# Optimization experiments

Hardware: AMD Instinct MI355X
Metric: run time of the kernel (lower is better)

The kernel has to match this reference:

```python
import jax, jax.numpy as jnp
import numpy as np

B, A = 8192, 16
HID, NK, NQ, NV = 256, 32, 32, 128
IN_DIM, CUR_HID, CUR_OUT, N_ACT = 512, 512, 128, 64
EXT_LAMBD, INT_LAMBD = 1.0, 0.5


def setup_inputs() -> dict:
    key = jax.random.key(0)
    ks = jax.random.split(key, 16)
    def w(k, i, o):
        return jax.random.normal(k, (i, o), jnp.float32) / np.sqrt(i)
    return {
        'x': jax.random.normal(ks[0], (B * A, IN_DIM), jnp.float32),
        'hidden': jax.random.normal(ks[1], (B, A, HID), jnp.float32),
        'Wk': w(ks[2], HID, NK), 'bk': jnp.zeros((NK,), jnp.float32),
        'Wv': w(ks[3], HID, NV), 'bv': jnp.zeros((NV,), jnp.float32),
        'Wq': w(ks[4], HID, NQ), 'bq': jnp.zeros((NQ,), jnp.float32),
        'Wa': w(ks[5], NQ + NK * A, A), 'ba': jnp.zeros((A,), jnp.float32),
        'Wt1': w(ks[6], IN_DIM, CUR_HID), 'bt1': jnp.zeros((CUR_HID,), jnp.float32),
        'Wt2': w(ks[7], CUR_HID, CUR_OUT), 'bt2': jnp.zeros((CUR_OUT,), jnp.float32),
        'Wp1': w(ks[8], IN_DIM, CUR_HID), 'bp1': jnp.zeros((CUR_HID,), jnp.float32),
        'Wp2': w(ks[9], CUR_HID, CUR_HID), 'bp2': jnp.zeros((CUR_HID,), jnp.float32),
        'Wp3': w(ks[10], CUR_HID, CUR_OUT), 'bp3': jnp.zeros((CUR_OUT,), jnp.float32),
        'Wc': w(ks[11], NV + HID, HID), 'bc': jnp.zeros((HID,), jnp.float32),
        'W2': w(ks[12], HID, N_ACT), 'b2': jnp.zeros((N_ACT,), jnp.float32),
    }


def _aggregate(x, hidden, Wk, bk, Wv, bv, Wq, bq, Wa, ba, Wt1, bt1, Wt2, bt2,
               Wp1, bp1, Wp2, bp2, Wp3, bp3, Wc, bc, W2, b2):
    # communicate(): per-agent key / value / query projections
    key_ = hidden @ Wk + bk          # [B, A, NK]
    value = hidden @ Wv + bv         # [B, A, NV]
    query = hidden @ Wq + bq         # [B, A, NQ]
    # torch.cat([key[:, i, :] for i in range(A)], -1) == reshape; repeat == broadcast
    flat_key = key_.reshape(B, A * NK)
    qk = jnp.concatenate(
        [query, jnp.broadcast_to(flat_key[:, None, :], (B, A, A * NK))], axis=-1)
    attn_weights = jax.nn.softmax(qk @ Wa + ba, axis=-1)   # [B, A, A]
    # intrinsic-motivation predictors (dropout p=0.5 in eval mode -> identity)
    tar = jax.nn.relu(x @ Wt1 + bt1) @ Wt2 + bt2           # [B*A, CUR_OUT]
    pred = jax.nn.relu(x @ Wp1 + bp1)
    pred = jax.nn.relu(pred @ Wp2 + bp2)
    pred = pred @ Wp3 + bp3
    int_imp = jnp.mean((tar - pred) ** 2, axis=-1).reshape(B, A)
    int_imp = jax.nn.softmax(int_imp, axis=-1)             # [B, A]
    # view(B,A,1).repeat(1,1,A).permute(0,2,1): out[b,i,j] = int_imp[b,j]
    int_mat = jnp.broadcast_to(int_imp[:, None, :], (B, A, A))
    attn = EXT_LAMBD * attn_weights + INT_LAMBD * jax.lax.stop_gradient(int_mat)
    applied = jnp.einsum('bij,bjv->biv', attn, value)      # [B, A, NV]
    comb = jax.nn.relu(jnp.concatenate([applied, hidden], axis=-1) @ Wc + bc)
    return comb @ W2 + b2                                  # [B, A, N_ACT]


def reference(x, hidden, Wk, bk, Wv, bv, Wq, bq, Wa, ba, Wt1, bt1, Wt2, bt2,
              Wp1, bp1, Wp2, bp2, Wp3, bp3, Wc, bc, W2, b2):
    return _aggregate(x, hidden, Wk, bk, Wv, bv, Wq, bq, Wa, ba, Wt1, bt1,
                      Wt2, bt2, Wp1, bp1, Wp2, bp2, Wp3, bp3, Wc, bc, W2, b2)
```

## Files before the change

### kernel.cpp

```cpp
#include <hip/hip_runtime.h>
#include <cstddef>
#include <cstdint>

typedef unsigned short ushort_t;
typedef __attribute__((ext_vector_type(4))) float f32x4;
typedef __attribute__((ext_vector_type(8))) short bf16x8;

#define BB   8192
#define AA   16
#define BA   131072

__device__ __forceinline__ float bf2f(ushort_t u) {
    union { float f; uint32_t i; } v; v.i = ((uint32_t)u) << 16; return v.f;
}
__device__ __forceinline__ ushort_t f2bf(float f) {
    union { float f; uint32_t i; } v; v.f = f;
    uint32_t r = v.i + 0x7fffu + ((v.i >> 16) & 1u);
    return (ushort_t)(r >> 16);
}
__device__ __forceinline__ void gload_lds16(const void* g, void* l) {
    __builtin_amdgcn_global_load_lds(
        (const __attribute__((address_space(1))) uint32_t*)g,
        (__attribute__((address_space(3))) uint32_t*)l, 16, 0, 0);
}

template<bool RELU>
__global__ __launch_bounds__(512, 2)
void gemm8p(const ushort_t* __restrict__ A, int lda,
            const ushort_t* __restrict__ A2, int lda2, int ksplit,
            const ushort_t* __restrict__ Bt,
            const float* __restrict__ bias,
            ushort_t* __restrict__ C, int ldc, int K, int lgx, int rpx)
{
    __shared__ ushort_t lds[65536];

    const int tid  = threadIdx.x;
    const int w    = tid >> 6;
    const int lane = tid & 63;
    const int wm   = w >> 2;
    const int wn   = w & 3;
    const int fr   = lane & 15;
    const int fq   = lane >> 4;

    const int bid  = blockIdx.x;
    const int xcd  = bid & 7;
    const int slot = bid >> 3;
    const int x    = slot & ((1 << lgx) - 1);
    const int y    = xcd * rpx + (slot >> lgx);
    const size_t brow = (size_t)y * 256;
    const int    bcol = x * 256;

    const int NT = K >> 6;
    const int NI = NT >> 1;

    const int srl = tid >> 3;
    const int spg = tid & 7;

    f32x4 acc[8][4];
#pragma unroll
    for (int m = 0; m < 8; ++m)
#pragma unroll
        for (int n = 0; n < 4; ++n) acc[m][n] = (f32x4){0.f, 0.f, 0.f, 0.f};

    auto stageA = [&](int T, int s, int bi) {
        const int k0  = T << 6;
        const int row = (srl < 32) ? s * 32 + srl : 128 + s * 32 + (srl - 32);
        const int col = ((spg ^ (row & 7)) << 3);
        const ushort_t* src;
        if (k0 >= ksplit) src = A2 + (brow + row) * (size_t)lda2 + (k0 - ksplit) + col;
        else              src = A  + (brow + row) * (size_t)lda  + k0 + col;
        gload_lds16(src, &lds[(bi << 15) + row * 64 + spg * 8]);
    };
    auto stageB = [&](int T, int c, int bi) {
        const int k0  = T << 6;
        const int row = c * 64 + srl;
        const int col = ((spg ^ (row & 7)) << 3);
        gload_lds16(Bt + (size_t)(bcol + row) * K + k0 + col,
                    &lds[(bi << 15) + 16384 + row * 64 + spg * 8]);
    };

    stageA(0, 0, 0); stageB(0, 0, 0);
    stageA(0, 1, 0); stageB(0, 1, 0);
    stageA(0, 2, 0); stageB(0, 2, 0);
    stageA(0, 3, 0); stageB(0, 3, 0);
    stageA(1, 0, 1); stageB(1, 0, 1);
    stageA(1, 1, 1); stageB(1, 1, 1);
    stageA(1, 2, 1); stageB(1, 2, 1);

    bf16x8 breg[4][2];

    for (int i = 0; i < NI; ++i) {
        const bool more = (i + 1 < NI);
#pragma unroll
        for (int h = 0; h < 2; ++h) {
            const int bufA = h << 15;
            const int bufB = (h << 15) + 16384;
#pragma unroll
            for (int q = 0; q < 4; ++q) {
                if (q == 0) {
                    if (h == 0 || more) asm volatile("s_waitcnt vmcnt(6)" ::: "memory");
                    else                asm volatile("s_waitcnt vmcnt(0)" ::: "memory");
                    __builtin_amdgcn_sched_barrier(0);
                    __builtin_amdgcn_s_barrier();
#pragma unroll
                    for (int n = 0; n < 4; ++n)
#pragma unroll
                        for (int kk = 0; kk < 2; ++kk) {
                            const int row = wn * 64 + n * 16 + fr;
                            const int gp  = ((kk * 4 + fq) ^ (row & 7)) << 3;
                            breg[n][kk] = *(const bf16x8*)&lds[bufB + row * 64 + gp];
                        }
                }
                bf16x8 areg[2][2];
#pragma unroll
                for (int j = 0; j < 2; ++j)
#pragma unroll
                    for (int kk = 0; kk < 2; ++kk) {
                        const int row = wm * 128 + (2 * q + j) * 16 + fr;
                        const int gp  = ((kk * 4 + fq) ^ (row & 7)) << 3;
                        areg[j][kk] = *(const bf16x8*)&lds[bufA + row * 64 + gp];
                    }
                if (h == 0) {
                    if (q == 0)      { stageA(2*i+1, 3, 1); stageB(2*i+1, 3, 1); }
                    else if (more)   { stageA(2*i+2, q-1, 0); stageB(2*i+2, q-1, 0); }
                } else {
                    if (q == 0) { if (more) { stageA(2*i+2, 3, 0); stageB(2*i+2, 3, 0); } }
                    else        { if (more) { stageA(2*i+3, q-1, 1); stageB(2*i+3, q-1, 1); } }
                }
                __builtin_amdgcn_s_barrier();
                __builtin_amdgcn_s_setprio(1);
#pragma unroll
                for (int j = 0; j < 2; ++j)
#pragma unroll
                    for (int n = 0; n < 4; ++n)
#pragma unroll
                        for (int kk = 0; kk < 2; ++kk)
                            acc[2*q+j][n] = __builtin_amdgcn_mfma_f32_16x16x32_bf16(
                                areg[j][kk], breg[n][kk], acc[2*q+j][n], 0, 0, 0);
                __builtin_amdgcn_s_setprio(0);
                __builtin_amdgcn_s_barrier();
            }
        }
    }

#pragma unroll
    for (int m = 0; m < 8; ++m) {
        const size_t rowb = brow + wm * 128 + m * 16 + fq * 4;
#pragma unroll
        for (int n = 0; n < 4; ++n) {
            const int col = bcol + wn * 64 + n * 16 + fr;
            const float bv = bias[col];
#pragma unroll
            for (int r = 0; r < 4; ++r) {
                float v = acc[m][n][r] + bv;
                if (RELU) v = fmaxf(v, 0.f);
                C[(rowb + r) * (size_t)ldc + col] = f2bf(v);
            }
        }
    }
}

template<bool OBF16, bool RELU>
__global__ __launch_bounds__(256)
void gemm_mfma(const ushort_t* __restrict__ A, int lda,
               const ushort_t* __restrict__ A2, int lda2, int ksplit,
               const ushort_t* __restrict__ Bt,
               const float* __restrict__ bias,
               void* __restrict__ C, int ldc, int N, int K, int lgx)
{
    __shared__ ushort_t As[2][128 * 64];
    __shared__ ushort_t Bs[2][128 * 64];

    const int tid  = threadIdx.x;
    const int w    = tid >> 6;
    const int lane = tid & 63;
    const int wm   = w >> 1;
    const int wn   = w & 1;

    const int bid  = blockIdx.x;
    const int xcd  = bid & 7;
    const int slot = bid >> 3;
    const int x    = slot & ((1 << lgx) - 1);
    const int y    = xcd * 128 + (slot >> lgx);
    const size_t brow = (size_t)y * 128;
    const int    bcol = x * 128;

    const int fr   = lane & 15;
    const int fq   = lane >> 4;
    const int srow = lane >> 3;
    const int scol = (lane & 7) << 3;

    f32x4 acc[4][4];
#pragma unroll
    for (int i = 0; i < 4; ++i)
#pragma unroll
        for (int j = 0; j < 4; ++j) acc[i][j] = (f32x4){0.f, 0.f, 0.f, 0.f};

    const int NT = K >> 6;

    auto stage = [&](int buf, int k0) {
#pragma unroll
        for (int i = 0; i < 4; ++i) {
            const int c = (w << 2) + i;
            const int r = (c << 3) + srow;
            const ushort_t* asrc;
            if (k0 >= ksplit)
                asrc = A2 + (brow + r) * (size_t)lda2 + (k0 - ksplit) + scol;
            else
                asrc = A  + (brow + r) * (size_t)lda  + k0 + scol;
            gload_lds16(asrc, &As[buf][(c << 9) + lane * 8]);
            gload_lds16(Bt + (size_t)(bcol + r) * K + k0 + scol,
                        &Bs[buf][(c << 9) + lane * 8]);
        }
    };

    stage(0, 0);
    __syncthreads();

    for (int t = 0; t < NT; ++t) {
        const int cur = t & 1;
        if (t + 1 < NT) stage(cur ^ 1, (t + 1) << 6);
#pragma unroll
        for (int kk = 0; kk < 2; ++kk) {
            bf16x8 a[4], b[4];
#pragma unroll
            for (int f = 0; f < 4; ++f) {
                a[f] = *(const bf16x8*)&As[cur][(wm * 64 + f * 16 + fr) * 64 + kk * 32 + fq * 8];
                b[f] = *(const bf16x8*)&Bs[cur][(wn * 64 + f * 16 + fr) * 64 + kk * 32 + fq * 8];
            }
#pragma unroll
            for (int fm = 0; fm < 4; ++fm)
#pragma unroll
                for (int fn = 0; fn < 4; ++fn)
                    acc[fm][fn] = __builtin_amdgcn_mfma_f32_16x16x32_bf16(
                        a[fm], b[fn], acc[fm][fn], 0, 0, 0);
        }
        __syncthreads();
    }

#pragma unroll
    for (int fm = 0; fm < 4; ++fm) {
        const size_t rowb = brow + wm * 64 + fm * 16 + fq * 4;
#pragma unroll
        for (int fn = 0; fn < 4; ++fn) {
            const int col = bcol + wn * 64 + fn * 16 + fr;
            if (col < N) {
                const float bv = bias[col];
#pragma unroll
                for (int r = 0; r < 4; ++r) {
                    float v = acc[fm][fn][r] + bv;
                    if (RELU) v = fmaxf(v, 0.f);
                    const size_t idx = (rowb + r) * (size_t)ldc + col;
                    if (OBF16) ((ushort_t*)C)[idx] = f2bf(v);
                    else       ((float*)C)[idx]    = v;
                }
            }
        }
    }
}

__global__ __launch_bounds__(256)
void transpose_w(const float* __restrict__ W, ushort_t* __restrict__ Wt,
                 int K, int N, int Npad)
{
    int idx = blockIdx.x * 256 + threadIdx.x;
    if (idx >= Npad * K) return;
    int n = idx / K, k = idx - n * K;
    float v = (n < N) ? W[(size_t)k * N + n] : 0.f;
    Wt[idx] = f2bf(v);
}

__global__ __launch_bounds__(256)
void transpose_wk(const float* __restrict__ W, ushort_t* __restrict__ Wt,
                  int Ksrc, int N, int ldk, int kOff, float sign)
{
    int idx = blockIdx.x * 256 + threadIdx.x;
    if (idx >= N * Ksrc) return;
    int n = idx / Ksrc, k = idx - n * Ksrc;
    Wt[(size_t)n * ldk + kOff + k] = f2bf(sign * W[(size_t)k * N + n]);
}

__global__ __launch_bounds__(256)
void conv_f32_bf16(const float* __restrict__ src, ushort_t* __restrict__ dst)
{
    size_t q = (size_t)blockIdx.x * 256 + threadIdx.x;
    float4 v = ((const float4*)src)[q];
    ushort_t* d = dst + q * 4;
    d[0] = f2bf(v.x); d[1] = f2bf(v.y); d[2] = f2bf(v.z); d[3] = f2bf(v.w);
}

__global__ __launch_bounds__(256)
void fill_zero(ushort_t* __restrict__ p, int n)
{
    int i = blockIdx.x * 256 + threadIdx.x;
    if (i < n) p[i] = 0;
}

__global__ void pack_cat2(const float* __restrict__ a, const float* __restrict__ b,
                          float* __restrict__ o)
{
    int j = blockIdx.x * 256 + threadIdx.x;
    if (j < 512) o[j] = a[j];
    else if (j < 1024) o[j] = b[j - 512];
}

__global__ void pack_bias(const float* __restrict__ bk, const float* __restrict__ bq,
                          const float* __restrict__ bv, float* __restrict__ pb)
{
    int j = threadIdx.x;
    float v = 0.f;
    if      (j < 32)  v = bk[j];
    else if (j < 64)  v = bq[j - 32];
    else if (j < 192) v = bv[j - 64];
    pb[j] = v;
}

__global__ void make_cbias(const float* __restrict__ bt2, const float* __restrict__ bp3,
                           float* __restrict__ cb)
{
    int j = threadIdx.x;
    cb[j] = (j < 128) ? (bt2[j] - bp3[j]) : 0.f;
}

__global__ __launch_bounds__(64)
void mse_softmax(const ushort_t* __restrict__ diff, float* __restrict__ int_imp)
{
    const int b = blockIdx.x, lane = threadIdx.x;
    __shared__ float m[AA];
    for (int a = 0; a < AA; ++a) {
        const uint32_t u = *(const uint32_t*)(diff + ((size_t)b * AA + a) * 256 + lane * 2);
        float d0 = bf2f((ushort_t)(u & 0xffff));
        float d1 = bf2f((ushort_t)(u >> 16));
        float s = d0 * d0 + d1 * d1;
#pragma unroll
        for (int off = 32; off > 0; off >>= 1) s += __shfl_down(s, off);
        if (lane == 0) m[a] = s * (1.f / 128.f);
    }
    __syncthreads();
    if (lane == 0) {
        float mx = -1e30f;
#pragma unroll
        for (int a = 0; a < AA; ++a) mx = fmaxf(mx, m[a]);
        float e[AA], den = 0.f;
#pragma unroll
        for (int a = 0; a < AA; ++a) { e[a] = __expf(m[a] - mx); den += e[a]; }
        float inv = 1.f / den;
#pragma unroll
        for (int a = 0; a < AA; ++a) int_imp[(size_t)b * AA + a] = e[a] * inv;
    }
}

__global__ __launch_bounds__(256)
void attn_apply(const ushort_t* __restrict__ kvq, const float* __restrict__ Wa,
                const float* __restrict__ ba, const float* __restrict__ iimp,
                ushort_t* __restrict__ applied)
{
    const int b = blockIdx.x, t = threadIdx.x;
    __shared__ float klds[512], qlds[512];
    __shared__ ushort_t vlds[2048];
    __shared__ float part[16][17];
    __shared__ float kp[16];
    __shared__ float attn[16][17];

    for (int i = t; i < 512; i += 256) {
        int a = i >> 5, c = i & 31;
        const size_t base = ((size_t)b * AA + a) * 256;
        klds[i] = bf2f(kvq[base + c]);
        qlds[i] = bf2f(kvq[base + 32 + c]);
    }
    for (int i = t; i < 2048; i += 256) {
        int j = i >> 7, v = i & 127;
        vlds[i] = kvq[((size_t)b * AA + j) * 256 + 64 + v];
    }
    __syncthreads();

    {
        int j = t & 15, seg = t >> 4;
        float s = 0.f;
        for (int c = seg * 32; c < seg * 32 + 32; ++c)
            s += klds[c] * Wa[(32 + c) * 16 + j];
        part[j][seg] = s;
    }
    __syncthreads();
    if (t < 16) {
        float s = 0.f;
#pragma unroll
        for (int seg = 0; seg < 16; ++seg) s += part[t][seg];
        kp[t] = s;
    }
    __syncthreads();

    {
        int i = t >> 4, j = t & 15;
        float s = 0.f;
#pragma unroll
        for (int q = 0; q < 32; ++q) s += qlds[i * 32 + q] * Wa[q * 16 + j];
        attn[i][j] = s + kp[j] + ba[j];
    }
    __syncthreads();
    if (t < 16) {
        float mx = -1e30f;
#pragma unroll
        for (int j = 0; j < 16; ++j) mx = fmaxf(mx, attn[t][j]);
        float e[16], den = 0.f;
#pragma unroll
        for (int j = 0; j < 16; ++j) { e[j] = __expf(attn[t][j] - mx); den += e[j]; }
        float inv = 1.f / den;
#pragma unroll
        for (int j = 0; j < 16; ++j)
            attn[t][j] = e[j] * inv + 0.5f * iimp[b * 16 + j];
    }
    __syncthreads();

    for (int o = t; o < 2048; o += 256) {
        int i = o >> 7, v = o & 127;
        float s = 0.f;
#pragma unroll
        for (int j = 0; j < 16; ++j) s += attn[i][j] * bf2f(vlds[j * 128 + v]);
        applied[((size_t)b * AA + i) * 128 + v] = f2bf(s);
    }
}

extern "C" void kernel_launch(void* const* d_in, const int* in_sizes, int n_in,
                              void* d_out, int out_size, void* d_ws, size_t ws_size,
                              hipStream_t stream)
{
    const float* x      = (const float*)d_in[0];
    const float* hidden = (const float*)d_in[1];
    const float* Wk  = (const float*)d_in[2];
    const float* bk  = (const float*)d_in[3];
    const float* Wv  = (const float*)d_in[4];
    const float* bv  = (const float*)d_in[5];
    const float* Wq  = (const float*)d_in[6];
    const float* bq  = (const float*)d_in[7];
    const float* Wa  = (const float*)d_in[8];
    const float* ba  = (const float*)d_in[9];
    const float* Wt1 = (const float*)d_in[10];
    const float* bt1 = (const float*)d_in[11];
    const float* Wt2 = (const float*)d_in[12];
    const float* bt2 = (const float*)d_in[13];
    const float* Wp1 = (const float*)d_in[14];
    const float* bp1 = (const float*)d_in[15];
    const float* Wp2 = (const float*)d_in[16];
    const float* bp2 = (const float*)d_in[17];
    const float* Wp3 = (const float*)d_in[18];
    const float* bp3 = (const float*)d_in[19];
    const float* Wc  = (const float*)d_in[20];
    const float* bc  = (const float*)d_in[21];
    const float* W2  = (const float*)d_in[22];
    const float* b2  = (const float*)d_in[23];

    float*    out = (float*)d_out;
    ushort_t* ws  = (ushort_t*)d_ws;

    ushort_t* xb  = ws;
    ushort_t* ht2 = xb + (size_t)BA * 512;
    ushort_t* hp2 = ht2 + (size_t)BA * 1024;
    ushort_t* WT  = hp2 + (size_t)BA * 512;
    ushort_t* diff    = xb;
    ushort_t* kvq     = xb + (size_t)BA * 256;
    ushort_t* hiddenb = hp2;
    ushort_t* applied = ht2;
    ushort_t* comb    = ht2 + (size_t)BA * 128;

    ushort_t* Bg1  = WT;
    ushort_t* Wp2t = Bg1  + 1024 * 512;
    ushort_t* Dt   = Wp2t + 512 * 512;
    ushort_t* Wkvq = Dt   + 256 * 1024;
    ushort_t* Wct  = Wkvq + 256 * 256;
    ushort_t* W2t  = Wct  + 256 * 384;
    float* g1bias = (float*)(W2t + 128 * 256);
    float* pbias  = g1bias + 1024;
    float* cbias  = pbias + 256;
    float* iimp   = cbias + 256;

    const dim3 blk(256);
    const int BIG = 1 << 30;

    transpose_w<<<1024, blk, 0, stream>>>(Wt1, Bg1,             512, 512, 512);
    transpose_w<<<1024, blk, 0, stream>>>(Wp1, Bg1 + 512 * 512, 512, 512, 512);
    transpose_w<<<1024, blk, 0, stream>>>(Wp2, Wp2t, 512, 512, 512);
    transpose_wk<<<256, blk, 0, stream>>>(Wt2, Dt, 512, 128, 1024, 0,    1.f);
    transpose_wk<<<256, blk, 0, stream>>>(Wp3, Dt, 512, 128, 1024, 512, -1.f);
    fill_zero<<<512, blk, 0, stream>>>(Dt + 128 * 1024, 128 * 1024);
    transpose_w<<<32,  blk, 0, stream>>>(Wk, Wkvq + 0 * 256,   256, 32, 32);
    transpose_w<<<32,  blk, 0, stream>>>(Wq, Wkvq + 32 * 256,  256, 32, 32);
    transpose_w<<<128, blk, 0, stream>>>(Wv, Wkvq + 64 * 256,  256, 128, 128);
    transpose_w<<<64,  blk, 0, stream>>>(Wk, Wkvq + 192 * 256, 256, 0, 64);
    transpose_w<<<384, blk, 0, stream>>>(Wc, Wct, 384, 256, 256);
    transpose_w<<<128, blk, 0, stream>>>(W2, W2t, 256, 64, 128);
    pack_cat2<<<4, 256, 0, stream>>>(bt1, bp1, g1bias);
    pack_bias<<<1, 256, 0, stream>>>(bk, bq, bv, pbias);
    make_cbias<<<1, 256, 0, stream>>>(bt2, bp3, cbias);

    conv_f32_bf16<<<65536, blk, 0, stream>>>(x, xb);
    gemm8p<true><<<2048, 512, 0, stream>>>(
        xb, 512, xb, 512, BIG, Bg1, g1bias, ht2, 1024, 512, 2, 64);
    gemm8p<true><<<1024, 512, 0, stream>>>(
        ht2 + 512, 1024, ht2 + 512, 1024, BIG, Wp2t, bp2, hp2, 512, 512, 1, 64);
    gemm8p<false><<<512, 512, 0, stream>>>(
        ht2, 1024, hp2, 512, 512, Dt, cbias, diff, 256, 1024, 0, 64);
    mse_softmax<<<BB, 64, 0, stream>>>(diff, iimp);

    conv_f32_bf16<<<32768, blk, 0, stream>>>(hidden, hiddenb);
    gemm8p<false><<<512, 512, 0, stream>>>(
        hiddenb, 256, hiddenb, 256, BIG, Wkvq, pbias, kvq, 256, 256, 0, 64);
    attn_apply<<<BB, blk, 0, stream>>>(kvq, Wa, ba, iimp, applied);

    gemm8p<true><<<512, 512, 0, stream>>>(
        applied, 128, hiddenb, 256, 128, Wct, bc, comb, 256, 384, 0, 64);
    gemm_mfma<false, false><<<1024, blk, 0, stream>>>(
        comb, 256, comb, 256, BIG, W2t, b2, out, 64, 64, 256, 0);
}
```

Baseline: 645.5 us.

## Fuse MSE-softmax and attention apply into GEMM epilogues

Adds epilogue modes to the 256x256 MFMA GEMM. One mode reduces the curiosity difference rows to squared-error means and applies the per-batch softmax inside the GEMM. The other keeps the K/Q/V tile in LDS, computes the attention logits, softmax and value mixing, and writes the applied tensor directly. This removes two standalone kernels and the global round-trips of the diff and kvq buffers. The cost is more LDS use and serial scalar epilogue work inside the GEMM blocks, and the launch-bounds occupancy hint is dropped.

```diff
diff --git a/kernel.cpp b/kernel.cpp
--- a/kernel.cpp
+++ b/kernel.cpp
@@ -24,13 +24,15 @@
         (__attribute__((address_space(3))) uint32_t*)l, 16, 0, 0);
 }
 
-template<bool RELU>
-__global__ __launch_bounds__(512, 2)
+template<int MODE, bool RELU>
+__global__ __launch_bounds__(512)
 void gemm8p(const ushort_t* __restrict__ A, int lda,
             const ushort_t* __restrict__ A2, int lda2, int ksplit,
             const ushort_t* __restrict__ Bt,
             const float* __restrict__ bias,
-            ushort_t* __restrict__ C, int ldc, int K, int lgx, int rpx)
+            ushort_t* __restrict__ C, int ldc, int K, int lgx, int rpx,
+            const float* __restrict__ Wa, const float* __restrict__ ba,
+            const float* __restrict__ iimp_in, float* __restrict__ iimp_out)
 {
     __shared__ ushort_t lds[65536];
 
@@ -143,18 +145,145 @@
         }
     }
 
-#pragma unroll
-    for (int m = 0; m < 8; ++m) {
-        const size_t rowb = brow + wm * 128 + m * 16 + fq * 4;
-#pragma unroll
-        for (int n = 0; n < 4; ++n) {
-            const int col = bcol + wn * 64 + n * 16 + fr;
-            const float bv = bias[col];
+    if (MODE == 0) {
+#pragma unroll
+        for (int m = 0; m < 8; ++m) {
+            const size_t rowb = brow + wm * 128 + m * 16 + fq * 4;
+#pragma unroll
+            for (int n = 0; n < 4; ++n) {
+                const int col = bcol + wn * 64 + n * 16 + fr;
+                const float bv = bias[col];
+#pragma unroll
+                for (int r = 0; r < 4; ++r) {
+                    float v = acc[m][n][r] + bv;
+                    if (RELU) v = fmaxf(v, 0.f);
+                    C[(rowb + r) * (size_t)ldc + col] = f2bf(v);
+                }
+            }
+        }
+    }
+
+    if (MODE == 1) {
+        float* rowsq = (float*)lds;
+        if (tid < 256) rowsq[tid] = 0.f;
+        __syncthreads();
+#pragma unroll
+        for (int m = 0; m < 8; ++m) {
 #pragma unroll
             for (int r = 0; r < 4; ++r) {
-                float v = acc[m][n][r] + bv;
-                if (RELU) v = fmaxf(v, 0.f);
-                C[(rowb + r) * (size_t)ldc + col] = f2bf(v);
+                float s = 0.f;
+#pragma unroll
+                for (int n = 0; n < 4; ++n) {
+                    const int col = wn * 64 + n * 16 + fr;
+                    const float v = acc[m][n][r] + bias[col];
+                    s += v * v;
+                }
+                s += __shfl_xor(s, 1);
+                s += __shfl_xor(s, 2);
+                s += __shfl_xor(s, 4);
+                s += __shfl_xor(s, 8);
+                if (fr == 0)
+                    atomicAdd(&rowsq[wm * 128 + m * 16 + fq * 4 + r], s);
+            }
+        }
+        __syncthreads();
+        if (tid < 16) {
+            const int rb = tid * 16;
+            float mv[16], mx = -1e30f;
+#pragma unroll
+            for (int a = 0; a < 16; ++a) {
+                mv[a] = rowsq[rb + a] * (1.f / 128.f);
+                mx = fmaxf(mx, mv[a]);
+            }
+            float e[16], den = 0.f;
+#pragma unroll
+            for (int a = 0; a < 16; ++a) { e[a] = __expf(mv[a] - mx); den += e[a]; }
+            const float inv = 1.f / den;
+            const size_t b = brow / 16 + tid;
+#pragma unroll
+            for (int a = 0; a < 16; ++a) iimp_out[b * 16 + a] = e[a] * inv;
+        }
+    }
+
+    if (MODE == 2) {
+        const int KSTR = 196;
+        ushort_t* kv    = lds;
+        float*    kp    = (float*)(lds + 50176);
+        float*    attnw = (float*)(lds + 50176 + 512);
+#pragma unroll
+        for (int m = 0; m < 8; ++m) {
+            const int row = wm * 128 + m * 16 + fq * 4;
+#pragma unroll
+            for (int n = 0; n < 4; ++n) {
+                const int col = wn * 64 + n * 16 + fr;
+                if (col < 192) {
+                    const float bv = bias[col];
+#pragma unroll
+                    for (int r = 0; r < 4; ++r)
+                        kv[(row + r) * KSTR + col] = f2bf(acc[m][n][r] + bv);
+                }
+            }
+        }
+        __syncthreads();
+
+        const int b  = tid >> 5;
+        const int tl = tid & 31;
+        const int rb = b * 16;
+
+        {
+            const int j = tl & 15, half = tl >> 4;
+            float s = 0.f;
+            for (int c = half * 256; c < half * 256 + 256; ++c) {
+                const int a = c >> 5, cc = c & 31;
+                s += bf2f(kv[(rb + a) * KSTR + cc]) * Wa[(32 + c) * 16 + j];
+            }
+            s += __shfl_down(s, 16);
+            if (half == 0) kp[b * 16 + j] = s;
+        }
+        __syncthreads();
+
+        if (tid < 256) {
+            const int b2 = tid >> 4, i = tid & 15, rb2 = b2 * 16;
+            float l[16];
+#pragma unroll
+            for (int j = 0; j < 16; ++j) l[j] = kp[b2 * 16 + j] + ba[j];
+            for (int qq = 0; qq < 32; ++qq) {
+                const float qv = bf2f(kv[(rb2 + i) * KSTR + 32 + qq]);
+#pragma unroll
+                for (int j = 0; j < 16; ++j) l[j] += qv * Wa[qq * 16 + j];
+            }
+            float mx = -1e30f;
+#pragma unroll
+            for (int j = 0; j < 16; ++j) mx = fmaxf(mx, l[j]);
+            float den = 0.f;
+#pragma unroll
+            for (int j = 0; j < 16; ++j) { l[j] = __expf(l[j] - mx); den += l[j]; }
+            const float inv = 1.f / den;
+            const size_t gb = brow / 16 + b2;
+#pragma unroll
+            for (int j = 0; j < 16; ++j)
+                attnw[(b2 * 16 + i) * 16 + j] = l[j] * inv + 0.5f * iimp_in[gb * 16 + j];
+        }
+        __syncthreads();
+
+        {
+            const int i  = tl >> 1;
+            const int hc = (tl & 1) * 64;
+            float aw[16];
+#pragma unroll
+            for (int j = 0; j < 16; ++j) aw[j] = attnw[(b * 16 + i) * 16 + j];
+            const size_t orow = (brow + rb + i) * (size_t)ldc;
+            for (int c0 = 0; c0 < 64; c0 += 4) {
+                float o0 = 0.f, o1 = 0.f, o2 = 0.f, o3 = 0.f;
+#pragma unroll
+                for (int j = 0; j < 16; ++j) {
+                    const ushort_t* vr = &kv[(rb + j) * KSTR + 64 + hc + c0];
+                    const float a0 = aw[j];
+                    o0 += a0 * bf2f(vr[0]); o1 += a0 * bf2f(vr[1]);
+                    o2 += a0 * bf2f(vr[2]); o3 += a0 * bf2f(vr[3]);
+                }
+                ushort_t pk[4] = { f2bf(o0), f2bf(o1), f2bf(o2), f2bf(o3) };
+                *(uint2*)&C[orow + hc + c0] = *(const uint2*)pk;
             }
         }
     }
@@ -320,105 +449,6 @@
 {
     int j = threadIdx.x;
     cb[j] = (j < 128) ? (bt2[j] - bp3[j]) : 0.f;
-}
-
-__global__ __launch_bounds__(64)
-void mse_softmax(const ushort_t* __restrict__ diff, float* __restrict__ int_imp)
-{
-    const int b = blockIdx.x, lane = threadIdx.x;
-    __shared__ float m[AA];
-    for (int a = 0; a < AA; ++a) {
-        const uint32_t u = *(const uint32_t*)(diff + ((size_t)b * AA + a) * 256 + lane * 2);
-        float d0 = bf2f((ushort_t)(u & 0xffff));
-        float d1 = bf2f((ushort_t)(u >> 16));
-        float s = d0 * d0 + d1 * d1;
-#pragma unroll
-        for (int off = 32; off > 0; off >>= 1) s += __shfl_down(s, off);
-        if (lane == 0) m[a] = s * (1.f / 128.f);
-    }
-    __syncthreads();
-    if (lane == 0) {
-        float mx = -1e30f;
-#pragma unroll
-        for (int a = 0; a < AA; ++a) mx = fmaxf(mx, m[a]);
-        float e[AA], den = 0.f;
-#pragma unroll
-        for (int a = 0; a < AA; ++a) { e[a] = __expf(m[a] - mx); den += e[a]; }
-        float inv = 1.f / den;
-#pragma unroll
-        for (int a = 0; a < AA; ++a) int_imp[(size_t)b * AA + a] = e[a] * inv;
-    }
-}
-
-__global__ __launch_bounds__(256)
-void attn_apply(const ushort_t* __restrict__ kvq, const float* __restrict__ Wa,
-                const float* __restrict__ ba, const float* __restrict__ iimp,
-                ushort_t* __restrict__ applied)
-{
-    const int b = blockIdx.x, t = threadIdx.x;
-    __shared__ float klds[512], qlds[512];
-    __shared__ ushort_t vlds[2048];
-    __shared__ float part[16][17];
-    __shared__ float kp[16];
-    __shared__ float attn[16][17];
-
-    for (int i = t; i < 512; i += 256) {
-        int a = i >> 5, c = i & 31;
-        const size_t base = ((size_t)b * AA + a) * 256;
-        klds[i] = bf2f(kvq[base + c]);
-        qlds[i] = bf2f(kvq[base + 32 + c]);
-    }
-    for (int i = t; i < 2048; i += 256) {
-        int j = i >> 7, v = i & 127;
-        vlds[i] = kvq[((size_t)b * AA + j) * 256 + 64 + v];
-    }
-    __syncthreads();
-
-    {
-        int j = t & 15, seg = t >> 4;
-        float s = 0.f;
-        for (int c = seg * 32; c < seg * 32 + 32; ++c)
-            s += klds[c] * Wa[(32 + c) * 16 + j];
-        part[j][seg] = s;
-    }
-    __syncthreads();
-    if (t < 16) {
-        float s = 0.f;
-#pragma unroll
-        for (int seg = 0; seg < 16; ++seg) s += part[t][seg];
-        kp[t] = s;
-    }
-    __syncthreads();
-
-    {
-        int i = t >> 4, j = t & 15;
-        float s = 0.f;
-#pragma unroll
-        for (int q = 0; q < 32; ++q) s += qlds[i * 32 + q] * Wa[q * 16 + j];
-        attn[i][j] = s + kp[j] + ba[j];
-    }
-    __syncthreads();
-    if (t < 16) {
-        float mx = -1e30f;
-#pragma unroll
-        for (int j = 0; j < 16; ++j) mx = fmaxf(mx, attn[t][j]);
-        float e[16], den = 0.f;
-#pragma unroll
-        for (int j = 0; j < 16; ++j) { e[j] = __expf(attn[t][j] - mx); den += e[j]; }
-        float inv = 1.f / den;
-#pragma unroll
-        for (int j = 0; j < 16; ++j)
-            attn[t][j] = e[j] * inv + 0.5f * iimp[b * 16 + j];
-    }
-    __syncthreads();
-
-    for (int o = t; o < 2048; o += 256) {
-        int i = o >> 7, v = o & 127;
-        float s = 0.f;
-#pragma unroll
-        for (int j = 0; j < 16; ++j) s += attn[i][j] * bf2f(vlds[j * 128 + v]);
-        applied[((size_t)b * AA + i) * 128 + v] = f2bf(s);
-    }
 }
 
 extern "C" void kernel_launch(void* const* d_in, const int* in_sizes, int n_in,
@@ -457,8 +487,6 @@
     ushort_t* ht2 = xb + (size_t)BA * 512;
     ushort_t* hp2 = ht2 + (size_t)BA * 1024;
     ushort_t* WT  = hp2 + (size_t)BA * 512;
-    ushort_t* diff    = xb;
-    ushort_t* kvq     = xb + (size_t)BA * 256;
     ushort_t* hiddenb = hp2;
     ushort_t* applied = ht2;
     ushort_t* comb    = ht2 + (size_t)BA * 128;
@@ -494,21 +522,24 @@
     make_cbias<<<1, 256, 0, stream>>>(bt2, bp3, cbias);
 
     conv_f32_bf16<<<65536, blk, 0, stream>>>(x, xb);
-    gemm8p<true><<<2048, 512, 0, stream>>>(
-        xb, 512, xb, 512, BIG, Bg1, g1bias, ht2, 1024, 512, 2, 64);
-    gemm8p<true><<<1024, 512, 0, stream>>>(
-        ht2 + 512, 1024, ht2 + 512, 1024, BIG, Wp2t, bp2, hp2, 512, 512, 1, 64);
-    gemm8p<false><<<512, 512, 0, stream>>>(
-        ht2, 1024, hp2, 512, 512, Dt, cbias, diff, 256, 1024, 0, 64);
-    mse_softmax<<<BB, 64, 0, stream>>>(diff, iimp);
+    gemm8p<0, true><<<2048, 512, 0, stream>>>(
+        xb, 512, xb, 512, BIG, Bg1, g1bias, ht2, 1024, 512, 2, 64,
+        nullptr, nullptr, nullptr, nullptr);
+    gemm8p<0, true><<<1024, 512, 0, stream>>>(
+        ht2 + 512, 1024, ht2 + 512, 1024, BIG, Wp2t, bp2, hp2, 512, 512, 1, 64,
+        nullptr, nullptr, nullptr, nullptr);
+    gemm8p<1, false><<<512, 512, 0, stream>>>(
+        ht2, 1024, hp2, 512, 512, Dt, cbias, nullptr, 0, 1024, 0, 64,
+        nullptr, nullptr, nullptr, iimp);
 
     conv_f32_bf16<<<32768, blk, 0, stream>>>(hidden, hiddenb);
-    gemm8p<false><<<512, 512, 0, stream>>>(
-        hiddenb, 256, hiddenb, 256, BIG, Wkvq, pbias, kvq, 256, 256, 0, 64);
-    attn_apply<<<BB, blk, 0, stream>>>(kvq, Wa, ba, iimp, applied);
-
-    gemm8p<true><<<512, 512, 0, stream>>>(
-        applied, 128, hiddenb, 256, 128, Wct, bc, comb, 256, 384, 0, 64);
+    gemm8p<2, false><<<512, 512, 0, stream>>>(
+        hiddenb, 256, hiddenb, 256, BIG, Wkvq, pbias, applied, 128, 256, 0, 64,
+        Wa, ba, iimp, nullptr);
+
+    gemm8p<0, true><<<512, 512, 0, stream>>>(
+        applied, 128, hiddenb, 256, 128, Wct, bc, comb, 256, 384, 0, 64,
+        nullptr, nullptr, nullptr, nullptr);
     gemm_mfma<false, false><<<1024, blk, 0, stream>>>(
         comb, 256, comb, 256, BIG, W2t, b2, out, 64, 64, 256, 0);
 }
```

Measured after the change: 690.6 us. 1.07x slower.

## Fuse MSE and softmax into diff GEMM epilogue and trim padded KVQ output

Applied to the files above, without the earlier changes.

The tar-minus-pred GEMM now runs on the 128x128 MFMA kernel with an MSE epilogue. It reduces squared row values in LDS and computes the per-batch softmax in place, so the bf16 diff tensor is never written and the separate mse_softmax kernel is gone. The zero-padded N=256 columns of the diff weights and the K/V/Q projection are dropped: KVQ is now stored with stride 192 through the smaller-tile MFMA kernel, with attention indexing changed to match. This cuts padding work, a global round trip and a launch, at the cost of LDS atomics in the epilogue and a smaller-tile GEMM for KVQ.

```diff
diff --git a/kernel.cpp b/kernel.cpp
--- a/kernel.cpp
+++ b/kernel.cpp
@@ -160,13 +160,14 @@
     }
 }
 
-template<bool OBF16, bool RELU>
+template<bool OBF16, bool RELU, bool MSE>
 __global__ __launch_bounds__(256)
 void gemm_mfma(const ushort_t* __restrict__ A, int lda,
                const ushort_t* __restrict__ A2, int lda2, int ksplit,
                const ushort_t* __restrict__ Bt,
                const float* __restrict__ bias,
-               void* __restrict__ C, int ldc, int N, int K, int lgx)
+               void* __restrict__ C, int ldc, int N, int K, int lgx,
+               float* __restrict__ iimp_out)
 {
     __shared__ ushort_t As[2][128 * 64];
     __shared__ ushort_t Bs[2][128 * 64];
@@ -238,6 +239,49 @@
         __syncthreads();
     }
 
+    if (MSE) {
+        float* rowsq = (float*)As;
+        if (tid < 128) rowsq[tid] = 0.f;
+        __syncthreads();
+#pragma unroll
+        for (int fm = 0; fm < 4; ++fm) {
+#pragma unroll
+            for (int r = 0; r < 4; ++r) {
+                float s = 0.f;
+#pragma unroll
+                for (int fn = 0; fn < 4; ++fn) {
+                    const int col = wn * 64 + fn * 16 + fr;
+                    const float v = acc[fm][fn][r] + bias[col];
+                    s += v * v;
+                }
+                s += __shfl_xor(s, 1);
+                s += __shfl_xor(s, 2);
+                s += __shfl_xor(s, 4);
+                s += __shfl_xor(s, 8);
+                if (fr == 0)
+                    atomicAdd(&rowsq[wm * 64 + fm * 16 + fq * 4 + r], s);
+            }
+        }
+        __syncthreads();
+        if (tid < 8) {
+            const int rb = tid * 16;
+            float mv[16], mx = -1e30f;
+#pragma unroll
+            for (int a = 0; a < 16; ++a) {
+                mv[a] = rowsq[rb + a] * (1.f / 128.f);
+                mx = fmaxf(mx, mv[a]);
+            }
+            float e[16], den = 0.f;
+#pragma unroll
+            for (int a = 0; a < 16; ++a) { e[a] = __expf(mv[a] - mx); den += e[a]; }
+            const float inv = 1.f / den;
+            const size_t b = brow / 16 + tid;
+#pragma unroll
+            for (int a = 0; a < 16; ++a) iimp_out[b * 16 + a] = e[a] * inv;
+        }
+        return;
+    }
+
 #pragma unroll
     for (int fm = 0; fm < 4; ++fm) {
         const size_t rowb = brow + wm * 64 + fm * 16 + fq * 4;
@@ -289,13 +333,6 @@
     d[0] = f2bf(v.x); d[1] = f2bf(v.y); d[2] = f2bf(v.z); d[3] = f2bf(v.w);
 }
 
-__global__ __launch_bounds__(256)
-void fill_zero(ushort_t* __restrict__ p, int n)
-{
-    int i = blockIdx.x * 256 + threadIdx.x;
-    if (i < n) p[i] = 0;
-}
-
 __global__ void pack_cat2(const float* __restrict__ a, const float* __restrict__ b,
                           float* __restrict__ o)
 {
@@ -319,35 +356,7 @@
                            float* __restrict__ cb)
 {
     int j = threadIdx.x;
-    cb[j] = (j < 128) ? (bt2[j] - bp3[j]) : 0.f;
-}
-
-__global__ __launch_bounds__(64)
-void mse_softmax(const ushort_t* __restrict__ diff, float* __restrict__ int_imp)
-{
-    const int b = blockIdx.x, lane = threadIdx.x;
-    __shared__ float m[AA];
-    for (int a = 0; a < AA; ++a) {
-        const uint32_t u = *(const uint32_t*)(diff + ((size_t)b * AA + a) * 256 + lane * 2);
-        float d0 = bf2f((ushort_t)(u & 0xffff));
-        float d1 = bf2f((ushort_t)(u >> 16));
-        float s = d0 * d0 + d1 * d1;
-#pragma unroll
-        for (int off = 32; off > 0; off >>= 1) s += __shfl_down(s, off);
-        if (lane == 0) m[a] = s * (1.f / 128.f);
-    }
-    __syncthreads();
-    if (lane == 0) {
-        float mx = -1e30f;
-#pragma unroll
-        for (int a = 0; a < AA; ++a) mx = fmaxf(mx, m[a]);
-        float e[AA], den = 0.f;
-#pragma unroll
-        for (int a = 0; a < AA; ++a) { e[a] = __expf(m[a] - mx); den += e[a]; }
-        float inv = 1.f / den;
-#pragma unroll
-        for (int a = 0; a < AA; ++a) int_imp[(size_t)b * AA + a] = e[a] * inv;
-    }
+    cb[j] = bt2[j] - bp3[j];
 }
 
 __global__ __launch_bounds__(256)
@@ -364,13 +373,13 @@
 
     for (int i = t; i < 512; i += 256) {
         int a = i >> 5, c = i & 31;
-        const size_t base = ((size_t)b * AA + a) * 256;
+        const size_t base = ((size_t)b * AA + a) * 192;
         klds[i] = bf2f(kvq[base + c]);
         qlds[i] = bf2f(kvq[base + 32 + c]);
     }
     for (int i = t; i < 2048; i += 256) {
         int j = i >> 7, v = i & 127;
-        vlds[i] = kvq[((size_t)b * AA + j) * 256 + 64 + v];
+        vlds[i] = kvq[((size_t)b * AA + j) * 192 + 64 + v];
     }
     __syncthreads();
 
@@ -457,8 +466,7 @@
     ushort_t* ht2 = xb + (size_t)BA * 512;
     ushort_t* hp2 = ht2 + (size_t)BA * 1024;
     ushort_t* WT  = hp2 + (size_t)BA * 512;
-    ushort_t* diff    = xb;
-    ushort_t* kvq     = xb + (size_t)BA * 256;
+    ushort_t* kvq     = xb;
     ushort_t* hiddenb = hp2;
     ushort_t* applied = ht2;
     ushort_t* comb    = ht2 + (size_t)BA * 128;
@@ -466,13 +474,13 @@
     ushort_t* Bg1  = WT;
     ushort_t* Wp2t = Bg1  + 1024 * 512;
     ushort_t* Dt   = Wp2t + 512 * 512;
-    ushort_t* Wkvq = Dt   + 256 * 1024;
+    ushort_t* Wkvq = Dt   + 128 * 1024;
     ushort_t* Wct  = Wkvq + 256 * 256;
     ushort_t* W2t  = Wct  + 256 * 384;
     float* g1bias = (float*)(W2t + 128 * 256);
     float* pbias  = g1bias + 1024;
     float* cbias  = pbias + 256;
-    float* iimp   = cbias + 256;
+    float* iimp   = cbias + 128;
 
     const dim3 blk(256);
     const int BIG = 1 << 30;
@@ -482,7 +490,6 @@
     transpose_w<<<1024, blk, 0, stream>>>(Wp2, Wp2t, 512, 512, 512);
     transpose_wk<<<256, blk, 0, stream>>>(Wt2, Dt, 512, 128, 1024, 0,    1.f);
     transpose_wk<<<256, blk, 0, stream>>>(Wp3, Dt, 512, 128, 1024, 512, -1.f);
-    fill_zero<<<512, blk, 0, stream>>>(Dt + 128 * 1024, 128 * 1024);
     transpose_w<<<32,  blk, 0, stream>>>(Wk, Wkvq + 0 * 256,   256, 32, 32);
     transpose_w<<<32,  blk, 0, stream>>>(Wq, Wkvq + 32 * 256,  256, 32, 32);
     transpose_w<<<128, blk, 0, stream>>>(Wv, Wkvq + 64 * 256,  256, 128, 128);
@@ -491,24 +498,23 @@
     transpose_w<<<128, blk, 0, stream>>>(W2, W2t, 256, 64, 128);
     pack_cat2<<<4, 256, 0, stream>>>(bt1, bp1, g1bias);
     pack_bias<<<1, 256, 0, stream>>>(bk, bq, bv, pbias);
-    make_cbias<<<1, 256, 0, stream>>>(bt2, bp3, cbias);
+    make_cbias<<<1, 128, 0, stream>>>(bt2, bp3, cbias);
 
     conv_f32_bf16<<<65536, blk, 0, stream>>>(x, xb);
     gemm8p<true><<<2048, 512, 0, stream>>>(
         xb, 512, xb, 512, BIG, Bg1, g1bias, ht2, 1024, 512, 2, 64);
     gemm8p<true><<<1024, 512, 0, stream>>>(
         ht2 + 512, 1024, ht2 + 512, 1024, BIG, Wp2t, bp2, hp2, 512, 512, 1, 64);
-    gemm8p<false><<<512, 512, 0, stream>>>(
-        ht2, 1024, hp2, 512, 512, Dt, cbias, diff, 256, 1024, 0, 64);
-    mse_softmax<<<BB, 64, 0, stream>>>(diff, iimp);
+    gemm_mfma<true, false, true><<<1024, blk, 0, stream>>>(
+        ht2, 1024, hp2, 512, 512, Dt, cbias, nullptr, 128, 128, 1024, 0, iimp);
 
     conv_f32_bf16<<<32768, blk, 0, stream>>>(hidden, hiddenb);
-    gemm8p<false><<<512, 512, 0, stream>>>(
-        hiddenb, 256, hiddenb, 256, BIG, Wkvq, pbias, kvq, 256, 256, 0, 64);
+    gemm_mfma<true, false, false><<<2048, blk, 0, stream>>>(
+        hiddenb, 256, hiddenb, 256, BIG, Wkvq, pbias, kvq, 192, 192, 256, 1, nullptr);
     attn_apply<<<BB, blk, 0, stream>>>(kvq, Wa, ba, iimp, applied);
 
     gemm8p<true><<<512, 512, 0, stream>>>(
         applied, 128, hiddenb, 256, 128, Wct, bc, comb, 256, 384, 0, 64);
-    gemm_mfma<false, false><<<1024, blk, 0, stream>>>(
-        comb, 256, comb, 256, BIG, W2t, b2, out, 64, 64, 256, 0);
-}
+    gemm_mfma<false, false, false><<<1024, blk, 0, stream>>>(
+        comb, 256, comb, 256, BIG, W2t, b2, out, 64, 64, 256, 0, nullptr);
+}
```

Measured after the change: 633.0 us. About the same (-1.9%).
